# Kernel optimization log

Measured on AMD Instinct MI355X. Metric: run time of the kernel, lower is better.

The kernel has to match this reference:

```python
import jax, jax.numpy as jnp
import numpy as np

V, D, NCTX, H, L, DM = 50257, 768, 1024, 12, 2, 3072
EPS = 1e-5
B, S = 2, 1024
DH = D // H


def _ln(x, w, b):
    # NOTE: faithful to source: divides by (std + eps), not sqrt(var + eps)
    m = jnp.mean(x, axis=-1, keepdims=True)
    std = jnp.sqrt(jnp.var(x, axis=-1, keepdims=True))
    return w * ((x - m) / (std + EPS)) + b


def setup_inputs() -> dict:
    key = jax.random.key(0)
    ks = jax.random.split(key, 20)
    r = 0.02
    inp = {
        "input_ids": jax.random.randint(ks[0], (B, S), 0, V),
        "embed": jax.random.normal(ks[1], (V, D), jnp.float32) * r,
        "pos_embed": jax.random.normal(ks[2], (NCTX, D), jnp.float32) * r,
        "ln1_w": jnp.ones((L, D)), "ln1_b": jnp.zeros((L, D)),
        "W_attn": jax.random.normal(ks[3], (L, 3 * D, D), jnp.float32) * r,
        "b_attn": jnp.zeros((L, 3 * D)),
        "W_O": jax.random.normal(ks[4], (L, D, D), jnp.float32) * r,
        "b_O": jnp.zeros((L, D)),
        "ln2_w": jnp.ones((L, D)), "ln2_b": jnp.zeros((L, D)),
        "W_in": jax.random.normal(ks[5], (L, DM, D), jnp.float32) * r,
        "b_in": jnp.zeros((L, DM)),
        "W_out": jax.random.normal(ks[6], (L, D, DM), jnp.float32) * r,
        "b_out": jnp.zeros((L, D)),
        "lnf_w": jnp.ones((D,)), "lnf_b": jnp.zeros((D,)),
        "W_U": jax.random.normal(ks[7], (V, D), jnp.float32) * r,
        "b_U": jnp.zeros((V,)),
    }
    return inp


def _forward(input_ids, embed, pos_embed, ln1_w, ln1_b, W_attn, b_attn, W_O, b_O,
             ln2_w, ln2_b, W_in, b_in, W_out, b_out, lnf_w, lnf_b, W_U, b_U):
    seq = input_ids.shape[1]
    res = embed[input_ids] + pos_embed[:seq][None, :, :]  # [B,S,D]
    causal = jnp.triu(jnp.ones((seq, seq), dtype=bool), 1)
    neg_inf = jnp.float32(-jnp.inf)
    for l in range(L):
        x = _ln(res, ln1_w[l], ln1_b[l])
        qkv = x @ W_attn[l].T + b_attn[l]  # [B,S,3D]
        q, k, v = jnp.split(qkv, 3, axis=-1)
        q = q.reshape(q.shape[0], seq, H, DH).transpose(0, 2, 1, 3)
        k = k.reshape(k.shape[0], seq, H, DH).transpose(0, 2, 1, 3)
        v = v.reshape(v.shape[0], seq, H, DH).transpose(0, 2, 1, 3)
        scores = jnp.einsum('bhqd,bhkd->bhqk', q, k) / (DH ** 0.5)
        scores = jnp.where(causal, neg_inf, scores)
        probs = jax.nn.softmax(scores, axis=-1)
        inter = jnp.einsum('bhqk,bhkd->bhqd', probs, v)
        inter = inter.transpose(0, 2, 1, 3).reshape(inter.shape[0], seq, D)
        res = inter @ W_O[l].T + b_O[l] + res
        y = _ln(res, ln2_w[l], ln2_b[l])
        h = jax.nn.gelu(y @ W_in[l].T + b_in[l], approximate=False)
        res = h @ W_out[l].T + b_out[l] + res
    res = _ln(res, lnf_w, lnf_b)
    return res @ W_U.T + b_U  # [B,S,V]


def reference(input_ids, embed, pos_embed, ln1_w, ln1_b, W_attn, b_attn, W_O, b_O,
              ln2_w, ln2_b, W_in, b_in, W_out, b_out, lnf_w, lnf_b, W_U, b_U):
    return _forward(input_ids, embed, pos_embed, ln1_w, ln1_b, W_attn, b_attn,
                    W_O, b_O, ln2_w, ln2_b, W_in, b_in, W_out, b_out,
                    lnf_w, lnf_b, W_U, b_U)
```

## Files before the change

### kernel.cpp

```cpp
#include <hip/hip_runtime.h>
#include <stdint.h>

#define D_MODEL 768
#define N_TOK   2048
#define SEQLEN  1024
#define N_HEAD  12
#define HEAD_D  64
#define N_LAYER 2
#define D_FF    3072
#define N_VOCAB 50257
#define D_QKV   2304

typedef unsigned short u16;
typedef __attribute__((ext_vector_type(8))) short bf16x8;
typedef __attribute__((ext_vector_type(4))) float f32x4;

__device__ __forceinline__ u16 f2b(float f) {
  uint32_t u = __float_as_uint(f);
  return (u16)((u + 0x7fffu + ((u >> 16) & 1u)) >> 16);
}
__device__ __forceinline__ float b2f(u16 h) {
  return __uint_as_float(((uint32_t)h) << 16);
}

__device__ __forceinline__ void gl2lds16(const void* g, void* l) {
  __builtin_amdgcn_global_load_lds(
      (const __attribute__((address_space(1))) uint32_t*)g,
      (__attribute__((address_space(3))) uint32_t*)l, 16, 0, 0);
}

__global__ __launch_bounds__(256) void cvt_k(const float* __restrict__ s,
                                             u16* __restrict__ d, int n4) {
  int i = blockIdx.x * 256 + threadIdx.x;
  if (i >= n4) return;
  float4 v = ((const float4*)s)[i];
  ushort4 o;
  o.x = f2b(v.x); o.y = f2b(v.y); o.z = f2b(v.z); o.w = f2b(v.w);
  ((ushort4*)d)[i] = o;
}

__global__ __launch_bounds__(256) void embed_k(const int* __restrict__ ids,
                                               const float* __restrict__ emb,
                                               const float* __restrict__ pos,
                                               float* __restrict__ R) {
  int t = blockIdx.x;
  int id = ids[t];
  int s = t & (SEQLEN - 1);
  const float* e = emb + (size_t)id * D_MODEL;
  const float* pp = pos + (size_t)s * D_MODEL;
  float* r = R + (size_t)t * D_MODEL;
  for (int i = threadIdx.x; i < D_MODEL; i += 256) r[i] = e[i] + pp[i];
}

__global__ __launch_bounds__(256) void ln_k(const float* __restrict__ X,
                                            const float* __restrict__ w,
                                            const float* __restrict__ b,
                                            u16* __restrict__ out) {
  int t = blockIdx.x;
  const float* x = X + (size_t)t * D_MODEL;
  float v0 = x[threadIdx.x], v1 = x[threadIdx.x + 256], v2 = x[threadIdx.x + 512];
  float s = v0 + v1 + v2;
  float s2 = v0 * v0 + v1 * v1 + v2 * v2;
  for (int off = 32; off; off >>= 1) {
    s  += __shfl_xor(s, off);
    s2 += __shfl_xor(s2, off);
  }
  __shared__ float rs[4], rq[4];
  int wv = threadIdx.x >> 6, ln = threadIdx.x & 63;
  if (ln == 0) { rs[wv] = s; rq[wv] = s2; }
  __syncthreads();
  s  = rs[0] + rs[1] + rs[2] + rs[3];
  s2 = rq[0] + rq[1] + rq[2] + rq[3];
  const float inv_d = 1.0f / (float)D_MODEL;
  float m = s * inv_d;
  float var = fmaxf(s2 * inv_d - m * m, 0.0f);
  float inv = 1.0f / (sqrtf(var) + 1e-5f);
  u16* o = out + (size_t)t * D_MODEL;
  int d0 = threadIdx.x;
  o[d0]       = f2b(w[d0]       * ((v0 - m) * inv) + b[d0]);
  o[d0 + 256] = f2b(w[d0 + 256] * ((v1 - m) * inv) + b[d0 + 256]);
  o[d0 + 512] = f2b(w[d0 + 512] * ((v2 - m) * inv) + b[d0 + 512]);
}

template <bool GELU, bool RES, bool OUT_BF16, bool VDUAL>
__global__ __launch_bounds__(256) void gemm_bt(
    const u16* __restrict__ A, const u16* __restrict__ B,
    const float* __restrict__ bias, const float* __restrict__ resid,
    void* __restrict__ Cout, u16* __restrict__ vtd, int M, int N, int K) {
  __shared__ u16 As[2][128 * 32];
  __shared__ u16 Bs[2][128 * 32];
  const int t = threadIdx.x;
  const int wv = t >> 6, ln = t & 63;
  const int wm = wv >> 1, wn = wv & 1;
  const int l15 = ln & 15, lq = ln >> 4;

  const int mtiles = M >> 7;
  const int nwg = gridDim.x;
  const int bid = blockIdx.x;
  const int qc = nwg >> 3, rc = nwg & 7;
  const int xcd = bid & 7, lid = bid >> 3;
  const int wgid = (xcd < rc ? xcd * (qc + 1) : rc * (qc + 1) + (xcd - rc) * qc) + lid;
  const int bm0 = (wgid % mtiles) * 128;
  const int bn0 = (wgid / mtiles) * 128;

  const int srow = wv * 32 + (ln >> 2);
  const int scol = (ln & 3) * 8;
  const u16* aS0 = A + (size_t)(bm0 + srow) * K + scol;
  const u16* aS1 = A + (size_t)(bm0 + srow + 16) * K + scol;
  int br0 = bn0 + srow;      if (br0 > N - 1) br0 = N - 1;
  int br1 = bn0 + srow + 16; if (br1 > N - 1) br1 = N - 1;
  const u16* bS0 = B + (size_t)br0 * K + scol;
  const u16* bS1 = B + (size_t)br1 * K + scol;

  f32x4 acc[4][4] = {};
  const int nk = K >> 5;

  gl2lds16(aS0, &As[0][wv * 1024]);
  gl2lds16(aS1, &As[0][wv * 1024 + 512]);
  gl2lds16(bS0, &Bs[0][wv * 1024]);
  gl2lds16(bS1, &Bs[0][wv * 1024 + 512]);
  __syncthreads();

  for (int kt = 0; kt < nk; ++kt) {
    const int cur = kt & 1;
    if (kt + 1 < nk) {
      const int ko = (kt + 1) << 5;
      const int nx = cur ^ 1;
      gl2lds16(aS0 + ko, &As[nx][wv * 1024]);
      gl2lds16(aS1 + ko, &As[nx][wv * 1024 + 512]);
      gl2lds16(bS0 + ko, &Bs[nx][wv * 1024]);
      gl2lds16(bS1 + ko, &Bs[nx][wv * 1024 + 512]);
    }
    bf16x8 af[4], bfr[4];
#pragma unroll
    for (int mi = 0; mi < 4; ++mi)
      af[mi] = *(const bf16x8*)&As[cur][(wm * 64 + mi * 16 + l15) * 32 + lq * 8];
#pragma unroll
    for (int ni = 0; ni < 4; ++ni)
      bfr[ni] = *(const bf16x8*)&Bs[cur][(wn * 64 + ni * 16 + l15) * 32 + lq * 8];
#pragma unroll
    for (int mi = 0; mi < 4; ++mi)
#pragma unroll
      for (int ni = 0; ni < 4; ++ni)
        acc[mi][ni] = __builtin_amdgcn_mfma_f32_16x16x32_bf16(af[mi], bfr[ni],
                                                              acc[mi][ni], 0, 0, 0);
    __syncthreads();
  }

#pragma unroll
  for (int ni = 0; ni < 4; ++ni) {
    int col = bn0 + wn * 64 + ni * 16 + l15;
    if (col >= N) continue;
    float bv = bias[col];
#pragma unroll
    for (int mi = 0; mi < 4; ++mi) {
      uint32_t vlo = 0, vhi = 0;
#pragma unroll
      for (int r = 0; r < 4; ++r) {
        int row = bm0 + wm * 64 + mi * 16 + lq * 4 + r;
        float v = acc[mi][ni][r] + bv;
        if constexpr (RES) v += resid[(size_t)row * N + col];
        if constexpr (GELU) v = 0.5f * v * (1.0f + erff(v * 0.70710678118f));
        if constexpr (OUT_BF16) {
          u16 hv = f2b(v);
          ((u16*)Cout)[(size_t)row * N + col] = hv;
          if constexpr (VDUAL) {
            if (r < 2) vlo |= ((uint32_t)hv) << (16 * r);
            else       vhi |= ((uint32_t)hv) << (16 * (r - 2));
          }
        } else {
          ((float*)Cout)[(size_t)row * N + col] = v;
        }
      }
      if constexpr (VDUAL) {
        if (col >= 2 * D_MODEL) {
          int row0 = bm0 + wm * 64 + mi * 16 + lq * 4;
          int bq = row0 >> 10, s = row0 & 1023;
          uint2 pk; pk.x = vlo; pk.y = vhi;
          *(uint2*)(vtd + (((size_t)bq * D_MODEL + (col - 2 * D_MODEL)) << 10) + s) = pk;
        }
      }
    }
  }
}

__global__ __launch_bounds__(256) void attn_mfma_k(const u16* __restrict__ qkv,
                                                   const u16* __restrict__ vt,
                                                   u16* __restrict__ out) {
  const int bh = blockIdx.y;
  const int b = bh / N_HEAD, h = bh % N_HEAD;
  const int qt = (gridDim.x - 1) - blockIdx.x;
  const int w = threadIdx.x >> 6, ln = threadIdx.x & 63;
  const int l15 = ln & 15, lq = ln >> 4;
  const int q0 = qt * 64;
  const int qb = q0 + w * 16;

  __shared__ u16 Plds[4][1024];
  char* pbase = (char*)&Plds[w][0];

  const u16* qp = qkv + ((size_t)(b * SEQLEN + qb + l15)) * D_QKV + h * HEAD_D + lq * 8;
  bf16x8 qf[2];
#pragma unroll
  for (int dk = 0; dk < 2; ++dk) {
    uint4 raw = *(const uint4*)(qp + dk * 32);
    const u16* pr = (const u16*)&raw;
    bf16x8 f;
#pragma unroll
    for (int j = 0; j < 8; ++j) f[j] = (short)f2b(b2f(pr[j]) * 0.125f);
    qf[dk] = f;
  }

  f32x4 oacc[4] = {};
  float mrun = -1e30f, lsum = 0.0f;
  const int qg = qb + l15;
  const int nch = qt + 1;

  const u16* kbase = qkv + (size_t)b * SEQLEN * D_QKV + D_MODEL + h * HEAD_D;
  const u16* vbase = vt + ((size_t)(bh * 64 + l15)) * SEQLEN;

  for (int c = 0; c < nch; ++c) {
    const int k0 = c * 64;
    bf16x8 kf[4][2];
#pragma unroll
    for (int mt = 0; mt < 4; ++mt)
#pragma unroll
      for (int dk = 0; dk < 2; ++dk)
        kf[mt][dk] = *(const bf16x8*)(kbase + (size_t)(k0 + mt * 16 + l15) * D_QKV +
                                      dk * 32 + lq * 8);
    f32x4 st[4] = {};
#pragma unroll
    for (int mt = 0; mt < 4; ++mt)
#pragma unroll
      for (int dk = 0; dk < 2; ++dk)
        st[mt] = __builtin_amdgcn_mfma_f32_16x16x32_bf16(kf[mt][dk], qf[dk],
                                                         st[mt], 0, 0, 0);
    if (k0 + 63 > qb) {
#pragma unroll
      for (int mt = 0; mt < 4; ++mt)
#pragma unroll
        for (int r = 0; r < 4; ++r) {
          int kg = k0 + mt * 16 + lq * 4 + r;
          if (kg > qg) st[mt][r] = -1e30f;
        }
    }
    float mc = -1e30f;
#pragma unroll
    for (int mt = 0; mt < 4; ++mt)
#pragma unroll
      for (int r = 0; r < 4; ++r) mc = fmaxf(mc, st[mt][r]);
    mc = fmaxf(mc, __shfl_xor(mc, 16));
    mc = fmaxf(mc, __shfl_xor(mc, 32));
    float mnew = fmaxf(mrun, mc);
    float pscale = __expf(mrun - mnew);
    mrun = mnew;
    float psum = 0.0f;
#pragma unroll
    for (int mt = 0; mt < 4; ++mt) {
      float p0 = __expf(st[mt][0] - mnew);
      float p1 = __expf(st[mt][1] - mnew);
      float p2 = __expf(st[mt][2] - mnew);
      float p3 = __expf(st[mt][3] - mnew);
      psum += (p0 + p1) + (p2 + p3);
      uint2 pk;
      pk.x = (uint32_t)f2b(p0) | ((uint32_t)f2b(p1) << 16);
      pk.y = (uint32_t)f2b(p2) | ((uint32_t)f2b(p3) << 16);
      int ow = (l15 * 128 + mt * 32 + lq * 8) ^ ((l15 & 7) << 4);
      *(uint2*)(pbase + ow) = pk;
    }
    lsum = lsum * pscale + psum;
    float ps0 = __shfl(pscale, lq * 4 + 0);
    float ps1 = __shfl(pscale, lq * 4 + 1);
    float ps2 = __shfl(pscale, lq * 4 + 2);
    float ps3 = __shfl(pscale, lq * 4 + 3);
#pragma unroll
    for (int nt = 0; nt < 4; ++nt) {
      oacc[nt][0] *= ps0; oacc[nt][1] *= ps1;
      oacc[nt][2] *= ps2; oacc[nt][3] *= ps3;
    }
#pragma unroll
    for (int kc = 0; kc < 2; ++kc) {
      int orr = (l15 * 128 + kc * 64 + lq * 16) ^ ((l15 & 7) << 4);
      bf16x8 pf = *(const bf16x8*)(pbase + orr);
#pragma unroll
      for (int nt = 0; nt < 4; ++nt) {
        bf16x8 vf = *(const bf16x8*)(vbase + (size_t)nt * 16 * SEQLEN +
                                     k0 + kc * 32 + lq * 8);
        oacc[nt] = __builtin_amdgcn_mfma_f32_16x16x32_bf16(pf, vf, oacc[nt], 0, 0, 0);
      }
    }
  }
  lsum += __shfl_xor(lsum, 16);
  lsum += __shfl_xor(lsum, 32);
  float inv = 1.0f / lsum;
  float i0 = __shfl(inv, lq * 4 + 0);
  float i1 = __shfl(inv, lq * 4 + 1);
  float i2 = __shfl(inv, lq * 4 + 2);
  float i3 = __shfl(inv, lq * 4 + 3);
  u16* ob = out + ((size_t)(b * SEQLEN + qb + lq * 4)) * D_MODEL + h * HEAD_D + l15;
#pragma unroll
  for (int nt = 0; nt < 4; ++nt) {
    ob[(size_t)0 * D_MODEL + nt * 16] = f2b(oacc[nt][0] * i0);
    ob[(size_t)1 * D_MODEL + nt * 16] = f2b(oacc[nt][1] * i1);
    ob[(size_t)2 * D_MODEL + nt * 16] = f2b(oacc[nt][2] * i2);
    ob[(size_t)3 * D_MODEL + nt * 16] = f2b(oacc[nt][3] * i3);
  }
}

extern "C" void kernel_launch(void* const* d_in, const int* in_sizes, int n_in,
                              void* d_out, int out_size, void* d_ws, size_t ws_size,
                              hipStream_t stream) {
  (void)in_sizes; (void)n_in; (void)out_size; (void)ws_size;
  const int*   ids   = (const int*)d_in[0];
  const float* emb   = (const float*)d_in[1];
  const float* pos   = (const float*)d_in[2];
  const float* ln1w  = (const float*)d_in[3];
  const float* ln1b  = (const float*)d_in[4];
  const float* Wattn = (const float*)d_in[5];
  const float* battn = (const float*)d_in[6];
  const float* WO    = (const float*)d_in[7];
  const float* bO    = (const float*)d_in[8];
  const float* ln2w  = (const float*)d_in[9];
  const float* ln2b  = (const float*)d_in[10];
  const float* Win   = (const float*)d_in[11];
  const float* bin   = (const float*)d_in[12];
  const float* Wout  = (const float*)d_in[13];
  const float* bout  = (const float*)d_in[14];
  const float* lnfw  = (const float*)d_in[15];
  const float* lnfb  = (const float*)d_in[16];
  const float* WU    = (const float*)d_in[17];
  const float* bU    = (const float*)d_in[18];

  char* p = (char*)d_ws;
  auto carve = [&](size_t bytes) {
    char* r = p;
    p += (bytes + 255) & ~(size_t)255;
    return r;
  };
  float* R      = (float*)carve((size_t)N_TOK * D_MODEL * 4);
  u16*   xb     = (u16*)carve((size_t)N_TOK * D_MODEL * 2);
  u16*   qkvb   = (u16*)carve((size_t)N_TOK * D_QKV * 2);
  u16*   attnb  = (u16*)carve((size_t)N_TOK * D_MODEL * 2);
  u16*   hb     = (u16*)carve((size_t)N_TOK * D_FF * 2);
  u16*   vtb    = (u16*)carve((size_t)2 * D_MODEL * SEQLEN * 2);
  u16*   Wattnb = (u16*)carve((size_t)N_LAYER * D_QKV * D_MODEL * 2);
  u16*   WOb    = (u16*)carve((size_t)N_LAYER * D_MODEL * D_MODEL * 2);
  u16*   Winb   = (u16*)carve((size_t)N_LAYER * D_FF * D_MODEL * 2);
  u16*   Woutb  = (u16*)carve((size_t)N_LAYER * D_MODEL * D_FF * 2);
  u16*   WUb    = (u16*)carve((size_t)N_VOCAB * D_MODEL * 2);

  auto cvt = [&](const float* s, u16* d, size_t n) {
    int n4 = (int)(n / 4);
    cvt_k<<<dim3((n4 + 255) / 256), dim3(256), 0, stream>>>(s, d, n4);
  };
  cvt(Wattn, Wattnb, (size_t)N_LAYER * D_QKV * D_MODEL);
  cvt(WO,    WOb,    (size_t)N_LAYER * D_MODEL * D_MODEL);
  cvt(Win,   Winb,   (size_t)N_LAYER * D_FF * D_MODEL);
  cvt(Wout,  Woutb,  (size_t)N_LAYER * D_MODEL * D_FF);
  cvt(WU,    WUb,    (size_t)N_VOCAB * D_MODEL);

  embed_k<<<dim3(N_TOK), dim3(256), 0, stream>>>(ids, emb, pos, R);

  const int MT = N_TOK / 128;
  for (int l = 0; l < N_LAYER; ++l) {
    ln_k<<<dim3(N_TOK), dim3(256), 0, stream>>>(R, ln1w + l * D_MODEL, ln1b + l * D_MODEL, xb);
    gemm_bt<false, false, true, true><<<dim3((D_QKV / 128) * MT), 256, 0, stream>>>(
        xb, Wattnb + (size_t)l * D_QKV * D_MODEL, battn + l * D_QKV, nullptr,
        qkvb, vtb, N_TOK, D_QKV, D_MODEL);
    attn_mfma_k<<<dim3(SEQLEN / 64, 2 * N_HEAD), 256, 0, stream>>>(qkvb, vtb, attnb);
    gemm_bt<false, true, false, false><<<dim3((D_MODEL / 128) * MT), 256, 0, stream>>>(
        attnb, WOb + (size_t)l * D_MODEL * D_MODEL, bO + l * D_MODEL, R,
        R, nullptr, N_TOK, D_MODEL, D_MODEL);
    ln_k<<<dim3(N_TOK), dim3(256), 0, stream>>>(R, ln2w + l * D_MODEL, ln2b + l * D_MODEL, xb);
    gemm_bt<true, false, true, false><<<dim3((D_FF / 128) * MT), 256, 0, stream>>>(
        xb, Winb + (size_t)l * D_FF * D_MODEL, bin + l * D_FF, nullptr,
        hb, nullptr, N_TOK, D_FF, D_MODEL);
    gemm_bt<false, true, false, false><<<dim3((D_MODEL / 128) * MT), 256, 0, stream>>>(
        hb, Woutb + (size_t)l * D_MODEL * D_FF, bout + l * D_MODEL, R,
        R, nullptr, N_TOK, D_MODEL, D_FF);
  }
  ln_k<<<dim3(N_TOK), dim3(256), 0, stream>>>(R, lnfw, lnfb, xb);
  gemm_bt<false, false, false, false><<<dim3(((N_VOCAB + 127) / 128) * MT), 256, 0, stream>>>(
      xb, WUb, bU, nullptr, d_out, nullptr, N_TOK, N_VOCAB, D_MODEL);
}
```

Baseline: 1.368 ms.

## Triple-buffer GEMM LDS pipeline with swizzled layout and coalesced fp32 epilogue

Moves the bf16 GEMM's LDS staging from double to triple buffering. Explicit vmcnt waits and raw barriers keep two tiles of global-to-LDS loads in flight while MFMAs run. The LDS layout gets an XOR swizzle to cut bank conflicts on the fragment reads, and MFMA issue priority is raised with s_setprio. For the plain fp32-output case (the vocab projection), the epilogue now transposes results through LDS so each wave writes full coalesced rows, instead of scattered 16-column strided stores. These changes add LDS footprint and hand-written waitcnt logic, which could lower occupancy or mis-synchronise if the count assumptions are wrong.

Measured after the change: 1.333 ms. 1.03x faster.

```diff
diff --git a/kernel.cpp b/kernel.cpp
--- a/kernel.cpp
+++ b/kernel.cpp
@@ -87,8 +87,8 @@
     const u16* __restrict__ A, const u16* __restrict__ B,
     const float* __restrict__ bias, const float* __restrict__ resid,
     void* __restrict__ Cout, u16* __restrict__ vtd, int M, int N, int K) {
-  __shared__ u16 As[2][128 * 32];
-  __shared__ u16 Bs[2][128 * 32];
+  __shared__ u16 As[3 * 4096];
+  __shared__ u16 Bs[3 * 4096];
   const int t = threadIdx.x;
   const int wv = t >> 6, ln = t & 63;
   const int wm = wv >> 1, wn = wv & 1;
@@ -104,80 +104,111 @@
   const int bn0 = (wgid / mtiles) * 128;
 
   const int srow = wv * 32 + (ln >> 2);
-  const int scol = (ln & 3) * 8;
-  const u16* aS0 = A + (size_t)(bm0 + srow) * K + scol;
-  const u16* aS1 = A + (size_t)(bm0 + srow + 16) * K + scol;
+  const int swz  = ((ln & 3) ^ ((ln >> 3) & 3)) * 8;
+  const u16* aS0 = A + (size_t)(bm0 + srow) * K + swz;
+  const u16* aS1 = A + (size_t)(bm0 + srow + 16) * K + swz;
   int br0 = bn0 + srow;      if (br0 > N - 1) br0 = N - 1;
   int br1 = bn0 + srow + 16; if (br1 > N - 1) br1 = N - 1;
-  const u16* bS0 = B + (size_t)br0 * K + scol;
-  const u16* bS1 = B + (size_t)br1 * K + scol;
+  const u16* bS0 = B + (size_t)br0 * K + swz;
+  const u16* bS1 = B + (size_t)br1 * K + swz;
 
   f32x4 acc[4][4] = {};
   const int nk = K >> 5;
 
-  gl2lds16(aS0, &As[0][wv * 1024]);
-  gl2lds16(aS1, &As[0][wv * 1024 + 512]);
-  gl2lds16(bS0, &Bs[0][wv * 1024]);
-  gl2lds16(bS1, &Bs[0][wv * 1024 + 512]);
-  __syncthreads();
-
+  auto stage = [&](int tile, int buf) {
+    const int ko = tile << 5;
+    u16* ab = &As[buf * 4096 + wv * 1024];
+    u16* bb = &Bs[buf * 4096 + wv * 1024];
+    gl2lds16(aS0 + ko, ab);
+    gl2lds16(aS1 + ko, ab + 512);
+    gl2lds16(bS0 + ko, bb);
+    gl2lds16(bS1 + ko, bb + 512);
+  };
+  stage(0, 0); stage(1, 1); stage(2, 2);
+
+  const int rsw = (lq ^ ((l15 >> 1) & 3)) * 8;
+  int cur = 0;
   for (int kt = 0; kt < nk; ++kt) {
-    const int cur = kt & 1;
-    if (kt + 1 < nk) {
-      const int ko = (kt + 1) << 5;
-      const int nx = cur ^ 1;
-      gl2lds16(aS0 + ko, &As[nx][wv * 1024]);
-      gl2lds16(aS1 + ko, &As[nx][wv * 1024 + 512]);
-      gl2lds16(bS0 + ko, &Bs[nx][wv * 1024]);
-      gl2lds16(bS1 + ko, &Bs[nx][wv * 1024 + 512]);
-    }
+    if (kt < nk - 2)       asm volatile("s_waitcnt vmcnt(8)" ::: "memory");
+    else if (kt == nk - 2) asm volatile("s_waitcnt vmcnt(4)" ::: "memory");
+    else                   asm volatile("s_waitcnt vmcnt(0)" ::: "memory");
+    __builtin_amdgcn_s_barrier();
+    const u16* ac = &As[cur * 4096];
+    const u16* bc = &Bs[cur * 4096];
     bf16x8 af[4], bfr[4];
 #pragma unroll
     for (int mi = 0; mi < 4; ++mi)
-      af[mi] = *(const bf16x8*)&As[cur][(wm * 64 + mi * 16 + l15) * 32 + lq * 8];
+      af[mi] = *(const bf16x8*)&ac[(wm * 64 + mi * 16 + l15) * 32 + rsw];
 #pragma unroll
     for (int ni = 0; ni < 4; ++ni)
-      bfr[ni] = *(const bf16x8*)&Bs[cur][(wn * 64 + ni * 16 + l15) * 32 + lq * 8];
+      bfr[ni] = *(const bf16x8*)&bc[(wn * 64 + ni * 16 + l15) * 32 + rsw];
+    __builtin_amdgcn_s_setprio(1);
 #pragma unroll
     for (int mi = 0; mi < 4; ++mi)
 #pragma unroll
       for (int ni = 0; ni < 4; ++ni)
         acc[mi][ni] = __builtin_amdgcn_mfma_f32_16x16x32_bf16(af[mi], bfr[ni],
                                                               acc[mi][ni], 0, 0, 0);
-    __syncthreads();
-  }
-
-#pragma unroll
-  for (int ni = 0; ni < 4; ++ni) {
-    int col = bn0 + wn * 64 + ni * 16 + l15;
-    if (col >= N) continue;
-    float bv = bias[col];
+    __builtin_amdgcn_s_setprio(0);
+    __builtin_amdgcn_s_barrier();
+    if (kt + 3 < nk) stage(kt + 3, cur);
+    cur = (cur == 2) ? 0 : cur + 1;
+  }
+
+  if constexpr (!OUT_BF16 && !RES && !GELU && !VDUAL) {
+    float* tr = ((float*)&As[0]) + wv * (16 * 65);
+    float* Cf = (float*)Cout;
 #pragma unroll
     for (int mi = 0; mi < 4; ++mi) {
-      uint32_t vlo = 0, vhi = 0;
-#pragma unroll
-      for (int r = 0; r < 4; ++r) {
-        int row = bm0 + wm * 64 + mi * 16 + lq * 4 + r;
-        float v = acc[mi][ni][r] + bv;
-        if constexpr (RES) v += resid[(size_t)row * N + col];
-        if constexpr (GELU) v = 0.5f * v * (1.0f + erff(v * 0.70710678118f));
-        if constexpr (OUT_BF16) {
-          u16 hv = f2b(v);
-          ((u16*)Cout)[(size_t)row * N + col] = hv;
-          if constexpr (VDUAL) {
-            if (r < 2) vlo |= ((uint32_t)hv) << (16 * r);
-            else       vhi |= ((uint32_t)hv) << (16 * (r - 2));
+#pragma unroll
+      for (int ni = 0; ni < 4; ++ni) {
+        int col = bn0 + wn * 64 + ni * 16 + l15;
+        float bv = (col < N) ? bias[col] : 0.0f;
+#pragma unroll
+        for (int r = 0; r < 4; ++r)
+          tr[(lq * 4 + r) * 65 + ni * 16 + l15] = acc[mi][ni][r] + bv;
+      }
+      int colw = bn0 + wn * 64 + ln;
+#pragma unroll
+      for (int r2 = 0; r2 < 16; ++r2) {
+        float v = tr[r2 * 65 + ln];
+        int row = bm0 + wm * 64 + mi * 16 + r2;
+        if (colw < N) Cf[(size_t)row * N + colw] = v;
+      }
+    }
+  } else {
+#pragma unroll
+    for (int ni = 0; ni < 4; ++ni) {
+      int col = bn0 + wn * 64 + ni * 16 + l15;
+      if (col >= N) continue;
+      float bv = bias[col];
+#pragma unroll
+      for (int mi = 0; mi < 4; ++mi) {
+        uint32_t vlo = 0, vhi = 0;
+#pragma unroll
+        for (int r = 0; r < 4; ++r) {
+          int row = bm0 + wm * 64 + mi * 16 + lq * 4 + r;
+          float v = acc[mi][ni][r] + bv;
+          if constexpr (RES) v += resid[(size_t)row * N + col];
+          if constexpr (GELU) v = 0.5f * v * (1.0f + erff(v * 0.70710678118f));
+          if constexpr (OUT_BF16) {
+            u16 hv = f2b(v);
+            ((u16*)Cout)[(size_t)row * N + col] = hv;
+            if constexpr (VDUAL) {
+              if (r < 2) vlo |= ((uint32_t)hv) << (16 * r);
+              else       vhi |= ((uint32_t)hv) << (16 * (r - 2));
+            }
+          } else {
+            ((float*)Cout)[(size_t)row * N + col] = v;
           }
-        } else {
-          ((float*)Cout)[(size_t)row * N + col] = v;
         }
-      }
-      if constexpr (VDUAL) {
-        if (col >= 2 * D_MODEL) {
-          int row0 = bm0 + wm * 64 + mi * 16 + lq * 4;
-          int bq = row0 >> 10, s = row0 & 1023;
-          uint2 pk; pk.x = vlo; pk.y = vhi;
-          *(uint2*)(vtd + (((size_t)bq * D_MODEL + (col - 2 * D_MODEL)) << 10) + s) = pk;
+        if constexpr (VDUAL) {
+          if (col >= 2 * D_MODEL) {
+            int row0 = bm0 + wm * 64 + mi * 16 + lq * 4;
+            int bq = row0 >> 10, s = row0 & 1023;
+            uint2 pk; pk.x = vlo; pk.y = vhi;
+            *(uint2*)(vtd + (((size_t)bq * D_MODEL + (col - 2 * D_MODEL)) << 10) + s) = pk;
+          }
         }
       }
     }
```
